# Kernel optimization log

Hardware: AMD Instinct MI355X
Metric: run time of the kernel (lower is better)

The kernel has to match this reference:

```python
import jax, jax.numpy as jnp
import numpy as np

F_BINS = 12
T_STEPS = 15
N = F_BINS * T_STEPS  # 180 patches
C = 768
R = C // 4            # 192 reduced dim for Q/K
B = 256
LN_EPS = 1e-5


def _build_physical_adjacency():
    A = np.zeros((N, N), dtype=np.float32)
    for f in range(F_BINS):
        for t in range(T_STEPS):
            i = f * T_STEPS + t
            if t < T_STEPS - 1:
                j = f * T_STEPS + (t + 1)
                A[i, j] = 1.0
                A[j, i] = 1.0
            hf = f * 2 + 1
            if hf < F_BINS:
                j = hf * T_STEPS + t
                A[i, j] = 1.0
                A[j, i] = 1.0
    A = A / (A.sum(axis=1, keepdims=True) + 1e-8)
    return jnp.asarray(A)


def setup_inputs() -> dict:
    key = jax.random.key(0)
    ks = jax.random.split(key, 8)
    x = jax.random.normal(ks[0], (B, N, C), dtype=jnp.float32)
    Wq = jax.random.normal(ks[1], (C, R), dtype=jnp.float32) * 0.02
    bq = jnp.zeros((R,), dtype=jnp.float32)
    Wk = jax.random.normal(ks[2], (C, R), dtype=jnp.float32) * 0.02
    bk = jnp.zeros((R,), dtype=jnp.float32)
    Wg = jax.random.normal(ks[3], (C, C), dtype=jnp.float32) * 0.02
    bg = jnp.zeros((C,), dtype=jnp.float32)
    gamma = jnp.ones((C,), dtype=jnp.float32)
    beta = jnp.zeros((C,), dtype=jnp.float32)
    alpha = jnp.asarray(0.8, dtype=jnp.float32)
    A_phys = _build_physical_adjacency()
    return {"x": x, "Wq": Wq, "bq": bq, "Wk": Wk, "bk": bk,
            "Wg": Wg, "bg": bg, "gamma": gamma, "beta": beta,
            "alpha": alpha, "A_phys": A_phys}


def reference(x, Wq, bq, Wk, bk, Wg, bg, gamma, beta, alpha, A_phys):
    # Q/K projections: [B,N,R]
    Q = jnp.einsum('bnc,cr->bnr', x, Wq) + bq
    K = jnp.einsum('bnc,cr->bnr', x, Wk) + bk
    # Dynamic adjacency: scaled dot-product softmax over nodes.
    scores = jnp.einsum('bnr,bmr->bnm', Q, K) / jnp.sqrt(jnp.asarray(R, x.dtype))
    A_dyn = jax.nn.softmax(scores, axis=-1)  # dropout is identity in eval
    a = jax.nn.sigmoid(alpha)
    A_comb = a * A_phys[None, :, :] + (1.0 - a) * A_dyn
    # GCN aggregation + projection
    z = jnp.einsum('bnm,bmc->bnc', A_comb, x)
    z = jnp.einsum('bnc,cd->bnd', z, Wg) + bg
    h = x + jax.nn.relu(z)
    # LayerNorm over channel dim
    mu = jnp.mean(h, axis=-1, keepdims=True)
    var = jnp.mean((h - mu) ** 2, axis=-1, keepdims=True)
    out = (h - mu) * jax.lax.rsqrt(var + LN_EPS) * gamma + beta
    return out
```

## Files before the change

kernel.cpp:

```cpp
#include <hip/hip_runtime.h>
#include <hip/hip_bf16.h>
#include <math.h>
#include <stdint.h>

#define BB   256
#define NN   180
#define CC   768
#define RR   192
#define MROWS (BB*NN)
#define KPAD 192

typedef __attribute__((ext_vector_type(8))) __bf16 bf16x8;
typedef __attribute__((ext_vector_type(4))) __bf16 bf16x4;
typedef __attribute__((ext_vector_type(4))) float  floatx4;

__device__ __forceinline__ void gload_lds16(const __bf16* g, __bf16* lds)
{
    __builtin_amdgcn_global_load_lds(
        (const __attribute__((address_space(1))) void*)(uintptr_t)(const void*)g,
        (__attribute__((address_space(3))) void*)(uintptr_t)(void*)lds,
        16, 0, 0);
}

template<int MODE>
__global__ __launch_bounds__(256) void gemm128(
    const __bf16* __restrict__ A,  int lda, long sAb,
    const __bf16* __restrict__ Bt, int ldb, long sBb,
    void* __restrict__ Cout, int ldc, long sCb,
    int M, int N, int K,
    const float* __restrict__ bias,
    const float* __restrict__ scale,
    const float* __restrict__ addx)
{
    const int z = blockIdx.z;
    const __bf16* Ab = A  + (long)z * sAb;
    const __bf16* Bb = Bt + (long)z * sBb;

    const int nwg = gridDim.x * gridDim.y;
    const int lin = blockIdx.y * gridDim.x + blockIdx.x;
    const int qd = nwg >> 3, rr = nwg & 7, xc = lin & 7, oo = lin >> 3;
    const int wg = (xc < rr ? xc * (qd + 1) : rr * (qd + 1) + (xc - rr) * qd) + oo;
    const int m0 = (wg / gridDim.x) * 128;
    const int n0 = (wg % gridDim.x) * 128;

    const int t  = threadIdx.x;
    const int w  = t >> 6;
    const int l  = t & 63;
    const int lr = l & 15;
    const int q  = l >> 4;
    const int xr = (lr >> 1) & 3;

    __shared__ __align__(16) __bf16 sa[2][128 * 32];
    __shared__ __align__(16) __bf16 sb[2][128 * 32];

    floatx4 acc[4][4] = {};

    const int wm = (w & 1) * 64;
    const int wn = (w >> 1) * 64;

    const int srow = l >> 2;
    const int skc  = ((l & 3) ^ ((l >> 3) & 3)) * 8;

    int arow0 = m0 + w * 16 + srow;        if (arow0 > M - 1) arow0 = M - 1;
    int arow1 = m0 + (w + 4) * 16 + srow;  if (arow1 > M - 1) arow1 = M - 1;
    int brow0 = n0 + w * 16 + srow;        if (brow0 > N - 1) brow0 = N - 1;
    int brow1 = n0 + (w + 4) * 16 + srow;  if (brow1 > N - 1) brow1 = N - 1;

    const __bf16* agp0 = Ab + (long)arow0 * lda + skc;
    const __bf16* agp1 = Ab + (long)arow1 * lda + skc;
    const __bf16* bgp0 = Bb + (long)brow0 * ldb + skc;
    const __bf16* bgp1 = Bb + (long)brow1 * ldb + skc;

    auto issue = [&](int buf, int k0) {
        gload_lds16(agp0 + k0, &sa[buf][(size_t)w * 512]);
        gload_lds16(agp1 + k0, &sa[buf][(size_t)(w + 4) * 512]);
        gload_lds16(bgp0 + k0, &sb[buf][(size_t)w * 512]);
        gload_lds16(bgp1 + k0, &sb[buf][(size_t)(w + 4) * 512]);
    };

    auto compute = [&](int buf) {
        bf16x8 af[4], bfv[4];
#pragma unroll
        for (int i = 0; i < 4; ++i)
            af[i] = *reinterpret_cast<const bf16x8*>(
                &sa[buf][(wm + i * 16 + lr) * 32 + ((q ^ xr) * 8)]);
#pragma unroll
        for (int j = 0; j < 4; ++j)
            bfv[j] = *reinterpret_cast<const bf16x8*>(
                &sb[buf][(wn + j * 16 + lr) * 32 + ((q ^ xr) * 8)]);
#pragma unroll
        for (int i = 0; i < 4; ++i)
#pragma unroll
            for (int j = 0; j < 4; ++j)
                acc[i][j] = __builtin_amdgcn_mfma_f32_16x16x32_bf16(af[i], bfv[j], acc[i][j], 0, 0, 0);
    };

    issue(0, 0);
    __syncthreads();
    for (int k0 = 0; k0 < K; k0 += 64) {
        issue(1, k0 + 32);
        compute(0);
        __syncthreads();
        if (k0 + 64 < K) issue(0, k0 + 64);
        compute(1);
        __syncthreads();
    }

#pragma unroll
    for (int i = 0; i < 4; ++i) {
        const int mbase = m0 + wm + i * 16 + q * 4;
#pragma unroll
        for (int j = 0; j < 4; ++j) {
            const int n = n0 + wn + j * 16 + lr;
#pragma unroll
            for (int r = 0; r < 4; ++r) {
                const int m = mbase + r;
                if (m < M && n < N) {
                    float v = acc[i][j][r];
                    if (MODE == 0) {
                        v = (v + bias[n]) * scale[n];
                        ((__bf16*)Cout)[(long)z * sCb + (long)m * ldc + n] = (__bf16)v;
                    } else if (MODE == 1) {
                        ((__bf16*)Cout)[(long)z * sCb + (long)m * ldc + n] = (__bf16)v;
                    } else {
                        v = v + bias[n];
                        v = v > 0.f ? v : 0.f;
                        v += addx[(long)m * ldc + n];
                        ((float*)Cout)[(long)m * ldc + n] = v;
                    }
                }
            }
        }
    }
}

__global__ __launch_bounds__(256) void convert_transpose_x(
    const float* __restrict__ x, __bf16* __restrict__ xb, __bf16* __restrict__ xbT)
{
    const int c0 = (blockIdx.x % 12) * 64;
    const int b  = blockIdx.x / 12;
    __shared__ __bf16 lds[64 * 194];
    const int t = threadIdx.x;

    for (int i = 0; i < 12; ++i) {
        int idx = i * 256 + t;
        if (idx < 2880) {
            int m = idx >> 4, c4 = idx & 15;
            float4 v = *reinterpret_cast<const float4*>(
                &x[((long)(b * NN + m)) * CC + c0 + c4 * 4]);
            bf16x4 o;
            o[0] = (__bf16)v.x; o[1] = (__bf16)v.y;
            o[2] = (__bf16)v.z; o[3] = (__bf16)v.w;
            *reinterpret_cast<bf16x4*>(&xb[((long)(b * NN + m)) * CC + c0 + c4 * 4]) = o;
            lds[(c4 * 4 + 0) * 194 + m] = o[0];
            lds[(c4 * 4 + 1) * 194 + m] = o[1];
            lds[(c4 * 4 + 2) * 194 + m] = o[2];
            lds[(c4 * 4 + 3) * 194 + m] = o[3];
        }
    }
    __syncthreads();
    for (int j = 0; j < 48; ++j) {
        int idx = j * 256 + t;
        int c = idx / KPAD, m = idx % KPAD;
        __bf16 v = (m < NN) ? lds[c * 194 + m] : (__bf16)0.0f;
        xbT[((long)(b * CC + c0 + c)) * KPAD + m] = v;
    }
}

__global__ __launch_bounds__(256) void prep_weights(
    const float* __restrict__ Wq, const float* __restrict__ bq,
    const float* __restrict__ Wk, const float* __restrict__ bk,
    const float* __restrict__ Wg,
    __bf16* __restrict__ WqkT, __bf16* __restrict__ WgT,
    float* __restrict__ biasqk, float* __restrict__ scaleqk)
{
    int blk = blockIdx.x, t = threadIdx.x;
    if (blk < 384) {
        int n = blk;
        const float* W = (n < RR) ? Wq : Wk;
        int nn = (n < RR) ? n : n - RR;
        for (int k = t; k < CC; k += 256)
            WqkT[(long)n * CC + k] = (__bf16)W[(long)k * RR + nn];
        if (blk == 0) {
            for (int i = t; i < 384; i += 256) {
                biasqk[i]  = (i < RR) ? bq[i] : bk[i - RR];
                scaleqk[i] = (i < RR) ? rsqrtf((float)RR) : 1.0f;
            }
        }
    } else {
        int n = blk - 384;
        for (int k = t; k < CC; k += 256)
            WgT[(long)n * CC + k] = (__bf16)Wg[(long)k * CC + n];
    }
}

__global__ __launch_bounds__(256) void softmax_combine(
    const __bf16* __restrict__ S, const float* __restrict__ A_phys,
    const float* __restrict__ alpha, __bf16* __restrict__ Acomb)
{
    const int w = threadIdx.x >> 6, l = threadIdx.x & 63;
    const long row = (long)blockIdx.x * 4 + w;
    const int b = (int)(row / NN), n = (int)(row % NN);
    const __bf16* Srow = S + ((long)b * NN + n) * NN;

    float v[3];
#pragma unroll
    for (int i = 0; i < 3; ++i) {
        int m = l + 64 * i;
        v[i] = (m < NN) ? (float)Srow[m] : -1e30f;
    }
    float mx = fmaxf(fmaxf(v[0], v[1]), v[2]);
    for (int off = 32; off; off >>= 1) mx = fmaxf(mx, __shfl_xor(mx, off, 64));

    float e[3], sum = 0.f;
#pragma unroll
    for (int i = 0; i < 3; ++i) {
        int m = l + 64 * i;
        e[i] = (m < NN) ? expf(v[i] - mx) : 0.f;
        sum += e[i];
    }
    for (int off = 32; off; off >>= 1) sum += __shfl_xor(sum, off, 64);

    const float a   = 1.f / (1.f + expf(-alpha[0]));
    const float inv = (1.f - a) / sum;
    __bf16* Orow = Acomb + ((long)b * NN + n) * KPAD;
#pragma unroll
    for (int i = 0; i < 3; ++i) {
        int m = l + 64 * i;
        if (m < KPAD) {
            float o = (m < NN) ? (a * A_phys[n * NN + m] + e[i] * inv) : 0.f;
            Orow[m] = (__bf16)o;
        }
    }
}

__global__ __launch_bounds__(256) void ln_kernel(float* __restrict__ out,
                                                 const float* __restrict__ gamma,
                                                 const float* __restrict__ beta)
{
    float* p = out + (long)blockIdx.x * CC;
    const int t = threadIdx.x, w = t >> 6, l = t & 63;
    float h[3], s = 0.f, s2 = 0.f;
#pragma unroll
    for (int i = 0; i < 3; ++i) {
        h[i] = p[t + 256 * i];
        s += h[i]; s2 += h[i] * h[i];
    }
    for (int off = 32; off; off >>= 1) { s += __shfl_xor(s, off, 64); s2 += __shfl_xor(s2, off, 64); }
    __shared__ float ps[4], ps2[4];
    if (l == 0) { ps[w] = s; ps2[w] = s2; }
    __syncthreads();
    s  = ps[0] + ps[1] + ps[2] + ps[3];
    s2 = ps2[0] + ps2[1] + ps2[2] + ps2[3];
    const float mu  = s * (1.f / CC);
    const float var = s2 * (1.f / CC) - mu * mu;
    const float rs  = rsqrtf(var + 1e-5f);
#pragma unroll
    for (int i = 0; i < 3; ++i) {
        int c = t + 256 * i;
        p[c] = (h[i] - mu) * rs * gamma[c] + beta[c];
    }
}

extern "C" void kernel_launch(void* const* d_in, const int* in_sizes, int n_in,
                              void* d_out, int out_size, void* d_ws, size_t ws_size,
                              hipStream_t stream)
{
    const float* x      = (const float*)d_in[0];
    const float* Wq     = (const float*)d_in[1];
    const float* bq     = (const float*)d_in[2];
    const float* Wk     = (const float*)d_in[3];
    const float* bk     = (const float*)d_in[4];
    const float* Wg     = (const float*)d_in[5];
    const float* bg     = (const float*)d_in[6];
    const float* gamma  = (const float*)d_in[7];
    const float* beta   = (const float*)d_in[8];
    const float* alpha  = (const float*)d_in[9];
    const float* A_phys = (const float*)d_in[10];

    char* w = (char*)d_ws;
    __bf16* xb    = (__bf16*)(w + 0);
    __bf16* zbuf  = xb;
    __bf16* xbT   = (__bf16*)(w + 70778880);
    __bf16* QK    = (__bf16*)(w + 146276352);
    __bf16* Acomb = QK;
    __bf16* S     = (__bf16*)(w + 181665792);
    __bf16* WqkT  = (__bf16*)(w + 198254592);
    __bf16* WgT   = (__bf16*)(w + 198844416);
    float*  biasqk  = (float*)(w + 200024064);
    float*  scaleqk = (float*)(w + 200025600);

    prep_weights<<<384 + CC, 256, 0, stream>>>(Wq, bq, Wk, bk, Wg, WqkT, WgT, biasqk, scaleqk);
    convert_transpose_x<<<BB * 12, 256, 0, stream>>>(x, xb, xbT);

    gemm128<0><<<dim3(384 / 128, MROWS / 128, 1), 256, 0, stream>>>(
        xb, CC, 0L, WqkT, CC, 0L, QK, 384, 0L,
        MROWS, 384, CC, biasqk, scaleqk, nullptr);

    gemm128<1><<<dim3(2, 2, BB), 256, 0, stream>>>(
        QK, 384, (long)NN * 384, QK + RR, 384, (long)NN * 384,
        S, NN, (long)NN * NN,
        NN, NN, RR, nullptr, nullptr, nullptr);

    softmax_combine<<<MROWS / 4, 256, 0, stream>>>(S, A_phys, alpha, Acomb);

    gemm128<1><<<dim3(CC / 128, 2, BB), 256, 0, stream>>>(
        Acomb, KPAD, (long)NN * KPAD, xbT, KPAD, (long)CC * KPAD,
        zbuf, CC, (long)NN * CC,
        NN, CC, KPAD, nullptr, nullptr, nullptr);

    gemm128<3><<<dim3(CC / 128, MROWS / 128, 1), 256, 0, stream>>>(
        zbuf, CC, 0L, WgT, CC, 0L, d_out, CC, 0L,
        MROWS, CC, CC, bg, nullptr, x);

    ln_kernel<<<MROWS, 256, 0, stream>>>((float*)d_out, gamma, beta);
}
```

Measured before the change: 667.2 us.

## Triple-buffer GEMM LDS tiles with explicit vmcnt waits and single barrier per chunk

Moves the templated bf16 MFMA GEMM from a double-buffered LDS pipeline with two __syncthreads per 64-wide K step to a three-slot ring buffer. Loads are issued two chunks ahead, and each chunk uses one partial s_waitcnt vmcnt plus one s_barrier. The aim is to keep more global loads in flight and cut barrier stalls. In exchange it uses 1.5x the LDS, which can lower occupancy. The ring also relies on the hand-written vmcnt counts being correct, since a wrong count would leave a hazard.

After: 666.5 us. No clear change (-0.1%).

```diff
diff --git a/kernel.cpp b/kernel.cpp
--- a/kernel.cpp
+++ b/kernel.cpp
@@ -50,8 +50,8 @@
     const int q  = l >> 4;
     const int xr = (lr >> 1) & 3;
 
-    __shared__ __align__(16) __bf16 sa[2][128 * 32];
-    __shared__ __align__(16) __bf16 sb[2][128 * 32];
+    __shared__ __align__(16) __bf16 sa[3][128 * 32];
+    __shared__ __align__(16) __bf16 sb[3][128 * 32];
 
     floatx4 acc[4][4] = {};
 
@@ -71,23 +71,24 @@
     const __bf16* bgp0 = Bb + (long)brow0 * ldb + skc;
     const __bf16* bgp1 = Bb + (long)brow1 * ldb + skc;
 
-    auto issue = [&](int buf, int k0) {
-        gload_lds16(agp0 + k0, &sa[buf][(size_t)w * 512]);
-        gload_lds16(agp1 + k0, &sa[buf][(size_t)(w + 4) * 512]);
-        gload_lds16(bgp0 + k0, &sb[buf][(size_t)w * 512]);
-        gload_lds16(bgp1 + k0, &sb[buf][(size_t)(w + 4) * 512]);
+    auto issue = [&](int slot, int cc) {
+        const int k0 = cc * 32;
+        gload_lds16(agp0 + k0, &sa[slot][(size_t)w * 512]);
+        gload_lds16(agp1 + k0, &sa[slot][(size_t)(w + 4) * 512]);
+        gload_lds16(bgp0 + k0, &sb[slot][(size_t)w * 512]);
+        gload_lds16(bgp1 + k0, &sb[slot][(size_t)(w + 4) * 512]);
     };
 
-    auto compute = [&](int buf) {
+    auto compute = [&](int slot) {
         bf16x8 af[4], bfv[4];
 #pragma unroll
         for (int i = 0; i < 4; ++i)
             af[i] = *reinterpret_cast<const bf16x8*>(
-                &sa[buf][(wm + i * 16 + lr) * 32 + ((q ^ xr) * 8)]);
+                &sa[slot][(wm + i * 16 + lr) * 32 + ((q ^ xr) * 8)]);
 #pragma unroll
         for (int j = 0; j < 4; ++j)
             bfv[j] = *reinterpret_cast<const bf16x8*>(
-                &sb[buf][(wn + j * 16 + lr) * 32 + ((q ^ xr) * 8)]);
+                &sb[slot][(wn + j * 16 + lr) * 32 + ((q ^ xr) * 8)]);
 #pragma unroll
         for (int i = 0; i < 4; ++i)
 #pragma unroll
@@ -95,15 +96,27 @@
                 acc[i][j] = __builtin_amdgcn_mfma_f32_16x16x32_bf16(af[i], bfv[j], acc[i][j], 0, 0, 0);
     };
 
+    const int NC = K >> 5;
+
     issue(0, 0);
-    __syncthreads();
-    for (int k0 = 0; k0 < K; k0 += 64) {
-        issue(1, k0 + 32);
-        compute(0);
-        __syncthreads();
-        if (k0 + 64 < K) issue(0, k0 + 64);
-        compute(1);
-        __syncthreads();
+    issue(1, 1);
+    asm volatile("s_waitcnt vmcnt(4)" ::: "memory");
+    __builtin_amdgcn_sched_barrier(0);
+    __builtin_amdgcn_s_barrier();
+    __builtin_amdgcn_sched_barrier(0);
+
+#pragma unroll 3
+    for (int c = 0; c < NC; ++c) {
+        const int cs = c % 3;
+        if (c + 2 < NC) issue((c + 2) % 3, c + 2);
+        compute(cs);
+        if (c + 1 < NC) {
+            if (c + 2 < NC) asm volatile("s_waitcnt vmcnt(4)" ::: "memory");
+            else            asm volatile("s_waitcnt vmcnt(0)" ::: "memory");
+            __builtin_amdgcn_sched_barrier(0);
+            __builtin_amdgcn_s_barrier();
+            __builtin_amdgcn_sched_barrier(0);
+        }
     }
 
 #pragma unroll
```
